# Kernel tuning notes

Measured on AMD Instinct MI355X. Metric: run time of the kernel, lower is better.

## Reference

```python
import jax, jax.numpy as jnp
import numpy as np

B, T, V, E, H, D1 = 4096, 255, 32000, 64, 64, 32

def setup_inputs() -> dict:
    key = jax.random.key(0)
    ks = jax.random.split(key, 6)
    return {
        "input_diffs": jax.random.randint(ks[0], (B, T), 0, V, dtype=jnp.int32),
        "embeddings": jax.random.normal(ks[1], (V, E), dtype=jnp.float32) * 0.1,
        "Wx": jax.random.normal(ks[2], (E, 4 * H), dtype=jnp.float32) * 0.1,
        "Wh": jax.random.normal(ks[3], (H, 4 * H), dtype=jnp.float32) * 0.1,
        "b_lstm": jnp.zeros((4 * H,), dtype=jnp.float32),
        "W1": jax.random.normal(ks[4], (E, D1), dtype=jnp.float32) * 0.1,
        "b1": jnp.zeros((D1,), dtype=jnp.float32),
        "W2": jax.random.normal(ks[5], (D1, V), dtype=jnp.float32) * 0.02,
        "b2": jnp.zeros((V,), dtype=jnp.float32),
    }

def _lstm_last(emb, Wx, Wh, b):
    # emb: [B, T, E] -> scan over time; Keras gate order i, f, c(g), o
    h0 = jnp.zeros((emb.shape[0], H), dtype=emb.dtype)
    c0 = jnp.zeros_like(h0)
    def step(carry, xt):
        h, c = carry
        z = xt @ Wx + h @ Wh + b                    # [B, 4H]
        i, f, g, o = jnp.split(z, 4, axis=-1)
        i = jax.nn.sigmoid(i); f = jax.nn.sigmoid(f)
        g = jnp.tanh(g);       o = jax.nn.sigmoid(o)
        c = f * c + i * g
        h = o * jnp.tanh(c)
        return (h, c), None
    (h, _), _ = jax.lax.scan(step, (h0, c0), jnp.swapaxes(emb, 0, 1))
    return h  # [B, H] (return_sequences=False)

def reference(input_diffs, embeddings, Wx, Wh, b_lstm, W1, b1, W2, b2):
    emb = embeddings[input_diffs]                   # [B, T, E] embedding lookup
    h = _lstm_last(emb, Wx, Wh, b_lstm)             # [B, H]
    out = jax.nn.relu(h @ W1 + b1)                  # [B, 32]
    logits = out @ W2 + b2                          # [B, V]
    return jax.nn.softmax(logits, axis=-1)
```

## Files before the change

### kernel.cpp

```cpp
#include <hip/hip_runtime.h>
#include <hip/hip_bf16.h>

#define B_  4096
#define T_  255
#define V_  32000
#define E_  64
#define H_  64
#define D1_ 32

#define NCT           2000
#define NCHUNK        10
#define CT_PER_CHUNK  200
#define CT_PER_WAVE   50

typedef __attribute__((ext_vector_type(8))) short bf16x8;
typedef __attribute__((ext_vector_type(4))) float f32x4;

__device__ __forceinline__ ushort f2bf(float f) {
    __hip_bfloat16 h = __float2bfloat16(f);
    return *reinterpret_cast<ushort*>(&h);
}
__device__ __forceinline__ float fast_sigmoid(float x) {
    return __builtin_amdgcn_rcpf(1.f + __expf(-x));
}
__device__ __forceinline__ float fast_tanh(float x) {
    return 1.f - 2.f * __builtin_amdgcn_rcpf(1.f + __expf(2.f * x));
}

__device__ __forceinline__ int hswz(int row, int colb) {
    return row * 128 + (colb ^ ((row & 7) << 4));
}

__global__ __launch_bounds__(256)
void emb2bf_kernel(const float* __restrict__ emb, ushort* __restrict__ emb_bf)
{
    int i = blockIdx.x * 256 + threadIdx.x;
    const float4 a = ((const float4*)emb)[i * 2];
    const float4 b = ((const float4*)emb)[i * 2 + 1];
    ushort t[8] = { f2bf(a.x), f2bf(a.y), f2bf(a.z), f2bf(a.w),
                    f2bf(b.x), f2bf(b.y), f2bf(b.z), f2bf(b.w) };
    *(ushort4*)(&emb_bf[i * 8])     = *(ushort4*)(&t[0]);
    *(ushort4*)(&emb_bf[i * 8 + 4]) = *(ushort4*)(&t[4]);
}

__global__ __launch_bounds__(256)
void lstm_mfma_kernel(const int* __restrict__ idx,
                      const ushort* __restrict__ emb_bf,
                      const float* __restrict__ Wx,
                      const float* __restrict__ Wh,
                      const float* __restrict__ b,
                      float* __restrict__ h_out)
{
    __shared__ __align__(16) char hbuf[2][2048];
    __shared__ int idxs[16 * 257];

    const int tid  = threadIdx.x;
    const int lane = tid & 63;
    const int w    = tid >> 6;
    const int r0   = blockIdx.x * 16;

    const int lrow = lane & 15;
    const int lhi  = lane >> 4;
    const int jcol = w * 16 + lrow;

    bf16x8 bw[16];
    float bias[4];
    #pragma unroll
    for (int g = 0; g < 4; ++g) {
        const int col = g * 64 + jcol;
        bias[g] = b[col];
        #pragma unroll
        for (int s = 0; s < 4; ++s) {
            bf16x8 f;
            #pragma unroll
            for (int i = 0; i < 8; ++i) {
                int k = s * 32 + lhi * 8 + i;
                float v = (k < 64) ? Wx[k * 256 + col] : Wh[(k - 64) * 256 + col];
                f[i] = (short)f2bf(v);
            }
            bw[g * 4 + s] = f;
        }
    }

    {
        const int row = tid >> 4, tc = tid & 15;
        #pragma unroll
        for (int k = 0; k < 16; ++k) {
            int t = k * 16 + tc;
            if (t < T_) idxs[row * 257 + t] = idx[(r0 + row) * T_ + t];
        }
        ((float2*)hbuf[0])[tid] = make_float2(0.f, 0.f);
    }
    __syncthreads();

    bf16x8 xc0, xc1, xn0, xn1;
    {
        int iv = idxs[lrow * 257 + 0];
        xc0 = *(const bf16x8*)(emb_bf + iv * 64 + lhi * 8);
        xc1 = *(const bf16x8*)(emb_bf + iv * 64 + 32 + lhi * 8);
        iv = idxs[lrow * 257 + 1];
        xn0 = *(const bf16x8*)(emb_bf + iv * 64 + lhi * 8);
        xn1 = *(const bf16x8*)(emb_bf + iv * 64 + 32 + lhi * 8);
    }

    float cst[4]  = {0.f, 0.f, 0.f, 0.f};
    float hreg[4] = {0.f, 0.f, 0.f, 0.f};

    for (int t = 0; t < T_; ++t) {
        const int p = t & 1;

        bf16x8 ah2 = *(const bf16x8*)(&hbuf[p][hswz(lrow, lhi * 16)]);
        bf16x8 ah3 = *(const bf16x8*)(&hbuf[p][hswz(lrow, 64 + lhi * 16)]);

        f32x4 z[4];
        #pragma unroll
        for (int g = 0; g < 4; ++g) z[g] = (f32x4){bias[g], bias[g], bias[g], bias[g]};
        #pragma unroll
        for (int g = 0; g < 4; ++g) z[g] = __builtin_amdgcn_mfma_f32_16x16x32_bf16(xc0, bw[g * 4 + 0], z[g], 0, 0, 0);
        #pragma unroll
        for (int g = 0; g < 4; ++g) z[g] = __builtin_amdgcn_mfma_f32_16x16x32_bf16(xc1, bw[g * 4 + 1], z[g], 0, 0, 0);
        #pragma unroll
        for (int g = 0; g < 4; ++g) z[g] = __builtin_amdgcn_mfma_f32_16x16x32_bf16(ah2, bw[g * 4 + 2], z[g], 0, 0, 0);
        #pragma unroll
        for (int g = 0; g < 4; ++g) z[g] = __builtin_amdgcn_mfma_f32_16x16x32_bf16(ah3, bw[g * 4 + 3], z[g], 0, 0, 0);

        xc0 = xn0; xc1 = xn1;
        if (t + 2 < T_) {
            int iv = idxs[lrow * 257 + (t + 2)];
            xn0 = *(const bf16x8*)(emb_bf + iv * 64 + lhi * 8);
            xn1 = *(const bf16x8*)(emb_bf + iv * 64 + 32 + lhi * 8);
        }

        #pragma unroll
        for (int r = 0; r < 4; ++r) {
            float cn = fast_sigmoid(z[1][r]) * cst[r]
                     + fast_sigmoid(z[0][r]) * fast_tanh(z[2][r]);
            cst[r] = cn;
            float hn = fast_sigmoid(z[3][r]) * fast_tanh(cn);
            hreg[r] = hn;
            const int row = lhi * 4 + r;
            *(ushort*)(&hbuf[p ^ 1][hswz(row, 2 * jcol)]) = f2bf(hn);
        }

        asm volatile("s_waitcnt lgkmcnt(0)\n\ts_barrier" ::: "memory");
    }

    #pragma unroll
    for (int r = 0; r < 4; ++r)
        h_out[(r0 + lhi * 4 + r) * H_ + jcol] = hreg[r];
}

__global__ __launch_bounds__(256)
void head1_kernel(const float* __restrict__ h,
                  const float* __restrict__ W1,
                  const float* __restrict__ b1,
                  ushort* __restrict__ out32bf)
{
    int i = blockIdx.x * 256 + threadIdx.x;
    int r = i >> 5, d = i & 31;
    float a = b1[d];
    #pragma unroll
    for (int k = 0; k < 64; ++k)
        a = fmaf(h[r * H_ + k], W1[k * D1_ + d], a);
    out32bf[i] = f2bf(fmaxf(a, 0.f));
}

__global__ __launch_bounds__(256)
void repack_w2_kernel(const float* __restrict__ W2, ushort* __restrict__ w2p)
{
    int t = blockIdx.x * 256 + threadIdx.x;
    if (t >= NCT * 64) return;
    int ct = t >> 6, l = t & 63;
    int kbase = (l >> 4) * 8, c = ct * 16 + (l & 15);
    ushort tmp[8];
    #pragma unroll
    for (int i = 0; i < 8; ++i)
        tmp[i] = f2bf(W2[(kbase + i) * V_ + c]);
    *(ushort4*)(&w2p[t * 8])     = *(ushort4*)(&tmp[0]);
    *(ushort4*)(&w2p[t * 8 + 4]) = *(ushort4*)(&tmp[4]);
}

template <int PASS>
__global__ __launch_bounds__(256)
void head2_mfma_kernel(const ushort* __restrict__ out32bf,
                       const ushort* __restrict__ w2p,
                       const float* __restrict__ b2,
                       float* __restrict__ partial,
                       float* __restrict__ out)
{
    __shared__ float red[4][16];
    __shared__ float sinvs[16];

    const int tid  = threadIdx.x;
    const int lane = tid & 63;
    const int w    = tid >> 6;
    const int lrow = lane & 15;
    const int lhi  = lane >> 4;
    const int r0    = blockIdx.x * 16;
    const int chunk = blockIdx.y;

    if (PASS == 2) {
        if (tid < 16) {
            float s = 0.f;
            #pragma unroll
            for (int c = 0; c < NCHUNK; ++c) s += partial[(r0 + tid) * NCHUNK + c];
            sinvs[tid] = 1.f / s;
        }
        __syncthreads();
    }

    const bf16x8 A = *(const bf16x8*)(out32bf + (r0 + lrow) * D1_ + lhi * 8);

    float sacc[4] = {0.f, 0.f, 0.f, 0.f};
    float si[4];
    if (PASS == 2) {
        #pragma unroll
        for (int r = 0; r < 4; ++r) si[r] = sinvs[lhi * 4 + r];
    }

    const int ct0 = chunk * CT_PER_CHUNK + w * CT_PER_WAVE;
    for (int i = 0; i < CT_PER_WAVE; ++i) {
        const int ct = ct0 + i;
        const bf16x8 Bf = *(const bf16x8*)(w2p + ct * 512 + lane * 8);
        f32x4 z = __builtin_amdgcn_mfma_f32_16x16x32_bf16(A, Bf, (f32x4){0.f, 0.f, 0.f, 0.f}, 0, 0, 0);
        const float b2v = b2[ct * 16 + lrow];
        #pragma unroll
        for (int r = 0; r < 4; ++r) {
            float e = __expf(z[r] + b2v);
            if (PASS == 1) sacc[r] += e;
            else out[(size_t)(r0 + lhi * 4 + r) * V_ + ct * 16 + lrow] = e * si[r];
        }
    }

    if (PASS == 1) {
        #pragma unroll
        for (int r = 0; r < 4; ++r) {
            float v = sacc[r];
            #pragma unroll
            for (int off = 1; off < 16; off <<= 1) v += __shfl_xor(v, off, 16);
            if (lrow == 0) red[w][lhi * 4 + r] = v;
        }
        __syncthreads();
        if (tid < 16)
            partial[(r0 + tid) * NCHUNK + chunk] =
                red[0][tid] + red[1][tid] + red[2][tid] + red[3][tid];
    }
}

extern "C" void kernel_launch(void* const* d_in, const int* in_sizes, int n_in,
                              void* d_out, int out_size, void* d_ws, size_t ws_size,
                              hipStream_t stream)
{
    (void)in_sizes; (void)n_in; (void)out_size; (void)ws_size;

    const int*   idx = (const int*)  d_in[0];
    const float* emb = (const float*)d_in[1];
    const float* Wx  = (const float*)d_in[2];
    const float* Wh  = (const float*)d_in[3];
    const float* bl  = (const float*)d_in[4];
    const float* W1  = (const float*)d_in[5];
    const float* b1  = (const float*)d_in[6];
    const float* W2  = (const float*)d_in[7];
    const float* b2  = (const float*)d_in[8];
    float* out = (float*)d_out;

    float*  ws      = (float*)d_ws;
    float*  h       = ws;
    ushort* out32bf = (ushort*)(ws + 262144);
    ushort* w2p     = (ushort*)(ws + 262144 + 65536);
    float*  part    = ws + 262144 + 65536 + 512000;
    ushort* emb_bf  = (ushort*)(ws + 262144 + 65536 + 512000 + 40960);

    emb2bf_kernel<<<(V_ * E_ / 8) / 256, 256, 0, stream>>>(emb, emb_bf);
    repack_w2_kernel<<<(NCT * 64 + 255) / 256, 256, 0, stream>>>(W2, w2p);
    lstm_mfma_kernel<<<256, 256, 0, stream>>>(idx, emb_bf, Wx, Wh, bl, h);
    head1_kernel<<<(B_ * D1_) / 256, 256, 0, stream>>>(h, W1, b1, out32bf);

    dim3 g3(B_ / 16, NCHUNK);
    head2_mfma_kernel<1><<<g3, 256, 0, stream>>>(out32bf, w2p, b2, part, out);
    head2_mfma_kernel<2><<<g3, 256, 0, stream>>>(out32bf, w2p, b2, part, out);
}
```

Measured before the change: 374.4 us.

## Precompute input-projection MFMAs one step ahead and merge prep kernels

The LSTM loop now computes the x@Wx part of the gate pre-activations for step t+2 during step t. It keeps two accumulator sets (even and odd steps) and prefetches embeddings four steps ahead. This takes half the MFMAs off the serial h-dependent critical path of each step, at the cost of more registers. The embedding bf16 conversion and the W2 repack are also merged into one launch to save a kernel launch.

```diff
diff --git a/kernel.cpp b/kernel.cpp
--- a/kernel.cpp
+++ b/kernel.cpp
@@ -32,15 +32,29 @@
 }
 
 __global__ __launch_bounds__(256)
-void emb2bf_kernel(const float* __restrict__ emb, ushort* __restrict__ emb_bf)
-{
-    int i = blockIdx.x * 256 + threadIdx.x;
-    const float4 a = ((const float4*)emb)[i * 2];
-    const float4 b = ((const float4*)emb)[i * 2 + 1];
-    ushort t[8] = { f2bf(a.x), f2bf(a.y), f2bf(a.z), f2bf(a.w),
-                    f2bf(b.x), f2bf(b.y), f2bf(b.z), f2bf(b.w) };
-    *(ushort4*)(&emb_bf[i * 8])     = *(ushort4*)(&t[0]);
-    *(ushort4*)(&emb_bf[i * 8 + 4]) = *(ushort4*)(&t[4]);
+void prep_kernel(const float* __restrict__ emb, ushort* __restrict__ emb_bf,
+                 const float* __restrict__ W2,  ushort* __restrict__ w2p)
+{
+    if (blockIdx.x < 1000) {
+        int i = blockIdx.x * 256 + threadIdx.x;
+        const float4 a = ((const float4*)emb)[i * 2];
+        const float4 b = ((const float4*)emb)[i * 2 + 1];
+        ushort t[8] = { f2bf(a.x), f2bf(a.y), f2bf(a.z), f2bf(a.w),
+                        f2bf(b.x), f2bf(b.y), f2bf(b.z), f2bf(b.w) };
+        *(ushort4*)(&emb_bf[i * 8])     = *(ushort4*)(&t[0]);
+        *(ushort4*)(&emb_bf[i * 8 + 4]) = *(ushort4*)(&t[4]);
+    } else {
+        int t = (blockIdx.x - 1000) * 256 + threadIdx.x;
+        if (t >= NCT * 64) return;
+        int ct = t >> 6, l = t & 63;
+        int kbase = (l >> 4) * 8, c = ct * 16 + (l & 15);
+        ushort tmp[8];
+        #pragma unroll
+        for (int i = 0; i < 8; ++i)
+            tmp[i] = f2bf(W2[(kbase + i) * V_ + c]);
+        *(ushort4*)(&w2p[t * 8])     = *(ushort4*)(&tmp[0]);
+        *(ushort4*)(&w2p[t * 8 + 4]) = *(ushort4*)(&tmp[4]);
+    }
 }
 
 __global__ __launch_bounds__(256)
@@ -58,7 +72,6 @@
     const int lane = tid & 63;
     const int w    = tid >> 6;
     const int r0   = blockIdx.x * 16;
-
     const int lrow = lane & 15;
     const int lhi  = lane >> 4;
     const int jcol = w * 16 + lrow;
@@ -93,42 +106,63 @@
     }
     __syncthreads();
 
-    bf16x8 xc0, xc1, xn0, xn1;
+    f32x4 zxe[4], zxo[4];
+    bf16x8 xe0, xe1, xo0, xo1;
     {
         int iv = idxs[lrow * 257 + 0];
-        xc0 = *(const bf16x8*)(emb_bf + iv * 64 + lhi * 8);
-        xc1 = *(const bf16x8*)(emb_bf + iv * 64 + 32 + lhi * 8);
+        bf16x8 a0 = *(const bf16x8*)(emb_bf + iv * 64 + lhi * 8);
+        bf16x8 a1 = *(const bf16x8*)(emb_bf + iv * 64 + 32 + lhi * 8);
+        #pragma unroll
+        for (int g = 0; g < 4; ++g) {
+            zxe[g] = (f32x4){bias[g], bias[g], bias[g], bias[g]};
+            zxe[g] = __builtin_amdgcn_mfma_f32_16x16x32_bf16(a0, bw[g * 4 + 0], zxe[g], 0, 0, 0);
+            zxe[g] = __builtin_amdgcn_mfma_f32_16x16x32_bf16(a1, bw[g * 4 + 1], zxe[g], 0, 0, 0);
+        }
         iv = idxs[lrow * 257 + 1];
-        xn0 = *(const bf16x8*)(emb_bf + iv * 64 + lhi * 8);
-        xn1 = *(const bf16x8*)(emb_bf + iv * 64 + 32 + lhi * 8);
+        a0 = *(const bf16x8*)(emb_bf + iv * 64 + lhi * 8);
+        a1 = *(const bf16x8*)(emb_bf + iv * 64 + 32 + lhi * 8);
+        #pragma unroll
+        for (int g = 0; g < 4; ++g) {
+            zxo[g] = (f32x4){bias[g], bias[g], bias[g], bias[g]};
+            zxo[g] = __builtin_amdgcn_mfma_f32_16x16x32_bf16(a0, bw[g * 4 + 0], zxo[g], 0, 0, 0);
+            zxo[g] = __builtin_amdgcn_mfma_f32_16x16x32_bf16(a1, bw[g * 4 + 1], zxo[g], 0, 0, 0);
+        }
+        iv = idxs[lrow * 257 + 2];
+        xe0 = *(const bf16x8*)(emb_bf + iv * 64 + lhi * 8);
+        xe1 = *(const bf16x8*)(emb_bf + iv * 64 + 32 + lhi * 8);
+        iv = idxs[lrow * 257 + 3];
+        xo0 = *(const bf16x8*)(emb_bf + iv * 64 + lhi * 8);
+        xo1 = *(const bf16x8*)(emb_bf + iv * 64 + 32 + lhi * 8);
     }
 
     float cst[4]  = {0.f, 0.f, 0.f, 0.f};
     float hreg[4] = {0.f, 0.f, 0.f, 0.f};
 
-    for (int t = 0; t < T_; ++t) {
+    auto do_step = [&](int t, f32x4* zx, bf16x8& x0, bf16x8& x1) {
         const int p = t & 1;
-
         bf16x8 ah2 = *(const bf16x8*)(&hbuf[p][hswz(lrow, lhi * 16)]);
         bf16x8 ah3 = *(const bf16x8*)(&hbuf[p][hswz(lrow, 64 + lhi * 16)]);
 
         f32x4 z[4];
         #pragma unroll
-        for (int g = 0; g < 4; ++g) z[g] = (f32x4){bias[g], bias[g], bias[g], bias[g]};
-        #pragma unroll
-        for (int g = 0; g < 4; ++g) z[g] = __builtin_amdgcn_mfma_f32_16x16x32_bf16(xc0, bw[g * 4 + 0], z[g], 0, 0, 0);
-        #pragma unroll
-        for (int g = 0; g < 4; ++g) z[g] = __builtin_amdgcn_mfma_f32_16x16x32_bf16(xc1, bw[g * 4 + 1], z[g], 0, 0, 0);
-        #pragma unroll
-        for (int g = 0; g < 4; ++g) z[g] = __builtin_amdgcn_mfma_f32_16x16x32_bf16(ah2, bw[g * 4 + 2], z[g], 0, 0, 0);
-        #pragma unroll
-        for (int g = 0; g < 4; ++g) z[g] = __builtin_amdgcn_mfma_f32_16x16x32_bf16(ah3, bw[g * 4 + 3], z[g], 0, 0, 0);
-
-        xc0 = xn0; xc1 = xn1;
+        for (int g = 0; g < 4; ++g)
+            z[g] = __builtin_amdgcn_mfma_f32_16x16x32_bf16(ah2, bw[g * 4 + 2], zx[g], 0, 0, 0);
+        #pragma unroll
+        for (int g = 0; g < 4; ++g)
+            z[g] = __builtin_amdgcn_mfma_f32_16x16x32_bf16(ah3, bw[g * 4 + 3], z[g], 0, 0, 0);
+
         if (t + 2 < T_) {
-            int iv = idxs[lrow * 257 + (t + 2)];
-            xn0 = *(const bf16x8*)(emb_bf + iv * 64 + lhi * 8);
-            xn1 = *(const bf16x8*)(emb_bf + iv * 64 + 32 + lhi * 8);
+            #pragma unroll
+            for (int g = 0; g < 4; ++g) {
+                zx[g] = (f32x4){bias[g], bias[g], bias[g], bias[g]};
+                zx[g] = __builtin_amdgcn_mfma_f32_16x16x32_bf16(x0, bw[g * 4 + 0], zx[g], 0, 0, 0);
+                zx[g] = __builtin_amdgcn_mfma_f32_16x16x32_bf16(x1, bw[g * 4 + 1], zx[g], 0, 0, 0);
+            }
+        }
+        if (t + 4 < T_) {
+            int iv = idxs[lrow * 257 + (t + 4)];
+            x0 = *(const bf16x8*)(emb_bf + iv * 64 + lhi * 8);
+            x1 = *(const bf16x8*)(emb_bf + iv * 64 + 32 + lhi * 8);
         }
 
         #pragma unroll
@@ -143,7 +177,13 @@
         }
 
         asm volatile("s_waitcnt lgkmcnt(0)\n\ts_barrier" ::: "memory");
-    }
+    };
+
+    for (int t = 0; t + 1 < T_; t += 2) {
+        do_step(t,     zxe, xe0, xe1);
+        do_step(t + 1, zxo, xo0, xo1);
+    }
+    do_step(T_ - 1, zxe, xe0, xe1);
 
     #pragma unroll
     for (int r = 0; r < 4; ++r)
@@ -163,21 +203,6 @@
     for (int k = 0; k < 64; ++k)
         a = fmaf(h[r * H_ + k], W1[k * D1_ + d], a);
     out32bf[i] = f2bf(fmaxf(a, 0.f));
-}
-
-__global__ __launch_bounds__(256)
-void repack_w2_kernel(const float* __restrict__ W2, ushort* __restrict__ w2p)
-{
-    int t = blockIdx.x * 256 + threadIdx.x;
-    if (t >= NCT * 64) return;
-    int ct = t >> 6, l = t & 63;
-    int kbase = (l >> 4) * 8, c = ct * 16 + (l & 15);
-    ushort tmp[8];
-    #pragma unroll
-    for (int i = 0; i < 8; ++i)
-        tmp[i] = f2bf(W2[(kbase + i) * V_ + c]);
-    *(ushort4*)(&w2p[t * 8])     = *(ushort4*)(&tmp[0]);
-    *(ushort4*)(&w2p[t * 8 + 4]) = *(ushort4*)(&tmp[4]);
 }
 
 template <int PASS>
@@ -271,8 +296,7 @@
     float*  part    = ws + 262144 + 65536 + 512000;
     ushort* emb_bf  = (ushort*)(ws + 262144 + 65536 + 512000 + 40960);
 
-    emb2bf_kernel<<<(V_ * E_ / 8) / 256, 256, 0, stream>>>(emb, emb_bf);
-    repack_w2_kernel<<<(NCT * 64 + 255) / 256, 256, 0, stream>>>(W2, w2p);
+    prep_kernel<<<1500, 256, 0, stream>>>(emb, emb_bf, W2, w2p);
     lstm_mfma_kernel<<<256, 256, 0, stream>>>(idx, emb_bf, Wx, Wh, bl, h);
     head1_kernel<<<(B_ * D1_) / 256, 256, 0, stream>>>(h, W1, b1, out32bf);
 
```

After: 360.1 us. -3.8%, faster.
